# Kernel tuning notes

Hardware: AMD Instinct MI355X
Metric: run time of the kernel (lower is better)

The kernel has to match this reference:

```python
import jax, jax.numpy as jnp
import numpy as np

B, T, D = 2, 2048, 1024
K, F = 8, 4096
LAMBDA = 0.5


def setup_inputs() -> dict:
    key = jax.random.key(0)
    ks = jax.random.split(key, 8)
    s = 0.02
    return {
        "x": jax.random.normal(ks[0], (B, T, D), dtype=jnp.float32),
        "prev_logits": jax.random.normal(ks[1], (B, T, K), dtype=jnp.float32),
        "Wt": jax.random.normal(ks[2], (D, K), dtype=jnp.float32) * s,
        "Wgt": jax.random.normal(ks[3], (K, K), dtype=jnp.float32) * s,
        "We_logits": jnp.zeros((K,), dtype=jnp.float32),
        "W1": jax.random.normal(ks[4], (K, D, F), dtype=jnp.float32) * s,
        "b1": jnp.zeros((K, F), dtype=jnp.float32),
        "W2": jax.random.normal(ks[5], (K, F, D), dtype=jnp.float32) * s,
        "b2": jnp.zeros((K, D), dtype=jnp.float32),
    }


def reference(x, prev_logits, Wt, Wgt, We_logits, W1, b1, W2, b2):
    # gating: softmax over router logits, sigmoid-threshold multi-hot mask
    logits = jnp.einsum("btd,dk->btk", x, Wt) + jnp.einsum("btk,kj->btj", prev_logits, Wgt)
    st = jax.nn.softmax(logits, axis=-1)                       # (B,T,K)
    We = jax.nn.sigmoid(We_logits)                             # (K,)
    mask = (st > LAMBDA * We).astype(x.dtype)                  # (B,T,K)
    g = st * mask
    sel_counts = mask.sum(axis=(0, 1))                         # (K,)
    avg_density = mask.sum(axis=-1).mean()                     # scalar

    # dense multi-expert FFN: every expert on every token (dropout=0 / eval)
    h = jax.nn.gelu(jnp.einsum("btd,kdf->bktf", x, W1) + b1[:, None, :], approximate=False)
    outk = jnp.einsum("bktf,kfd->bktd", h, W2) + b2[:, None, :]  # (B,K,T,D)
    y = jnp.einsum("btk,bktd->btd", g, outk)
    y = y / (g.sum(axis=-1, keepdims=True) + 1e-6)
    return y, jax.lax.stop_gradient(logits), sel_counts, avg_density
```

## Files before the change

kernel.cpp:

```cpp
#include <hip/hip_runtime.h>
#include <cstdint>
#include <cstddef>

#define NB 2
#define NTT 2048
#define ND 1024
#define NK 8
#define NF 4096
#define NTOK (NB*NTT)
#define LAMBDA_C 0.5f

#define Y_SZ   (NTOK*ND)
#define LG_OFF Y_SZ
#define SC_OFF (LG_OFF + NTOK*NK)
#define AD_OFF (SC_OFF + NK)

#define WS_CNT    0
#define WS_SEG    8
#define WS_NTILES 17
#define WS_TILEK  32
#define WS_TILER  1056
#define WS_PTOK   4096
#define WS_PCOEF  36864
#define WS_COEF   69632
#define WS_X16    102400
#define B_X16   409600ull
#define B_W1T   8798208ull
#define B_W2T   75907072ull
#define B_HBUFN 143015936ull
#define B_HBUFF 8798208ull

#define BM 128
#define BN 64
#define BK 64
#define SPLITK2 4
#define KT 16

#define AOFF0 0u
#define AOFF1 16384u
#define BOFF0 32768u
#define BOFF1 40960u

typedef float  f32x4 __attribute__((ext_vector_type(4)));
typedef _Float16 f16x8 __attribute__((ext_vector_type(8)));
typedef unsigned int u32x2 __attribute__((ext_vector_type(2)));
typedef unsigned int u32x4 __attribute__((ext_vector_type(4)));

__device__ __forceinline__ unsigned int pkrtz(float a, float b){
    auto h = __builtin_amdgcn_cvt_pkrtz(a, b);
    return __builtin_bit_cast(unsigned int, h);
}
__device__ __forceinline__ float gelu_exact(float v){
    return 0.5f * v * (1.0f + erff(v * 0.70710678118654752440f));
}

__global__ __launch_bounds__(256) void k_xcast(const float* __restrict__ x,
                                               unsigned short* __restrict__ x16)
{
    int i = (blockIdx.x*256 + threadIdx.x) * 16;
    const f32x4* src = (const f32x4*)(x + i);
    f32x4 v0 = src[0], v1 = src[1], v2 = src[2], v3 = src[3];
    u32x4 o0 = {pkrtz(v0[0],v0[1]), pkrtz(v0[2],v0[3]), pkrtz(v1[0],v1[1]), pkrtz(v1[2],v1[3])};
    u32x4 o1 = {pkrtz(v2[0],v2[1]), pkrtz(v2[2],v2[3]), pkrtz(v3[0],v3[1]), pkrtz(v3[2],v3[3])};
    *(u32x4*)(x16 + i)     = o0;
    *(u32x4*)(x16 + i + 8) = o1;
}

__global__ __launch_bounds__(256) void k_wtrans(
    const float* __restrict__ W1, const float* __restrict__ W2,
    unsigned short* __restrict__ W1T, unsigned short* __restrict__ W2T)
{
    __shared__ char LT[8192];
    int b = blockIdx.x;
    const float* src; unsigned short* dst; int sld, dld;
    if (b < 8192){
        int k = b >> 10, dt = (b >> 6) & 15, ft = b & 63;
        src = W1 + ((size_t)k*ND + dt*64)*NF + ft*64; sld = NF;
        dst = W1T + ((size_t)k*NF + ft*64)*ND + dt*64; dld = ND;
    } else {
        int b2 = b - 8192;
        int k = b2 >> 10, ft = (b2 >> 4) & 63, dt = b2 & 15;
        src = W2 + ((size_t)k*NF + ft*64)*ND + dt*64; sld = ND;
        dst = W2T + ((size_t)k*ND + dt*64)*NF + ft*64; dld = NF;
    }
    int t = threadIdx.x;
    int rg = t >> 4, cg = t & 15;
    f32x4 v[4];
    #pragma unroll
    for (int i = 0; i < 4; i++) v[i] = *(const f32x4*)(src + (size_t)(rg*4+i)*sld + cg*4);
    unsigned wA[4], wB[4];
    #pragma unroll
    for (int r = 0; r < 4; r++){
        wA[r] = pkrtz(v[r][0], v[r][1]);
        wB[r] = pkrtz(v[r][2], v[r][3]);
    }
    #pragma unroll
    for (int j = 0; j < 4; j++){
        unsigned s0 = (j < 2) ? wA[1] : wB[1];
        unsigned s1 = (j < 2) ? wA[0] : wB[0];
        unsigned s2 = (j < 2) ? wA[3] : wB[3];
        unsigned s3 = (j < 2) ? wA[2] : wB[2];
        unsigned sel = (j & 1) ? 0x07060302u : 0x05040100u;
        unsigned o0 = __builtin_amdgcn_perm(s0, s1, sel);
        unsigned o1 = __builtin_amdgcn_perm(s2, s3, sel);
        unsigned row_ = (unsigned)(cg*4 + j);
        unsigned g_ = ((unsigned)rg) ^ (2u*(row_ & 7u));
        *(u32x2*)(&LT[row_*128u + g_*8u]) = (u32x2){o0, o1};
    }
    __syncthreads();
    int c = t >> 2, ch = t & 3;
    unsigned sfx = (unsigned)c & 7u;
    unsigned p0 = ((unsigned)(2*ch))     ^ sfx;
    unsigned p1 = ((unsigned)(2*ch + 1)) ^ sfx;
    u32x4 r0 = *(const u32x4*)(&LT[(unsigned)c*128u + p0*16u]);
    u32x4 r1 = *(const u32x4*)(&LT[(unsigned)c*128u + p1*16u]);
    unsigned short* dp = dst + (size_t)c*dld + ch*16;
    *(u32x4*)(dp)     = r0;
    *(u32x4*)(dp + 8) = r1;
}

__global__ __launch_bounds__(256) void k_gating(
    const float* __restrict__ x, const float* __restrict__ pl,
    const float* __restrict__ Wt, const float* __restrict__ Wgt,
    const float* __restrict__ Wel, float* __restrict__ out,
    float* __restrict__ coef, int* __restrict__ cnt)
{
    int t = blockIdx.x;
    const float* xt = x + (size_t)t * ND;
    float acc[NK] = {0,0,0,0,0,0,0,0};
    for (int d = threadIdx.x; d < ND; d += 256){
        float xv = xt[d];
        const float4* w = (const float4*)(Wt + (size_t)d * NK);
        float4 w0 = w[0], w1 = w[1];
        acc[0] += xv*w0.x; acc[1] += xv*w0.y; acc[2] += xv*w0.z; acc[3] += xv*w0.w;
        acc[4] += xv*w1.x; acc[5] += xv*w1.y; acc[6] += xv*w1.z; acc[7] += xv*w1.w;
    }
    __shared__ float red[4][NK];
    #pragma unroll
    for (int k = 0; k < NK; k++){
        float v = acc[k];
        #pragma unroll
        for (int off = 32; off; off >>= 1) v += __shfl_down(v, off);
        if ((threadIdx.x & 63) == 0) red[threadIdx.x >> 6][k] = v;
    }
    __syncthreads();
    if (threadIdx.x == 0){
        const float* p = pl + (size_t)t * NK;
        float pv[NK];
        #pragma unroll
        for (int j = 0; j < NK; j++) pv[j] = p[j];
        float lg[NK]; float mx = -1e30f;
        #pragma unroll
        for (int k = 0; k < NK; k++){
            float v = red[0][k] + red[1][k] + red[2][k] + red[3][k];
            #pragma unroll
            for (int j = 0; j < NK; j++) v += pv[j] * Wgt[j*NK + k];
            lg[k] = v; mx = fmaxf(mx, v);
            out[LG_OFF + (size_t)t*NK + k] = v;
        }
        float e[NK]; float s = 0.f;
        #pragma unroll
        for (int k = 0; k < NK; k++){ e[k] = expf(lg[k] - mx); s += e[k]; }
        float g[NK]; float gsum = 0.f;
        #pragma unroll
        for (int k = 0; k < NK; k++){
            float st = e[k] / s;
            float we = 1.f / (1.f + expf(-Wel[k]));
            bool m = st > LAMBDA_C * we;
            g[k] = m ? st : 0.f;
            gsum += g[k];
        }
        float inv = 1.f / (gsum + 1e-6f);
        #pragma unroll
        for (int k = 0; k < NK; k++){
            coef[(size_t)t*NK + k] = g[k] * inv;
            if (g[k] > 0.f) atomicAdd(&cnt[k], 1);
        }
    }
}

__global__ __launch_bounds__(256) void k_scan(
    const float* __restrict__ coef, int* __restrict__ wsi,
    float* __restrict__ wsf, int pair_cap)
{
    int k = blockIdx.x;
    const int* cnt = wsi + WS_CNT;
    int base = 0;
    for (int j = 0; j < k; j++) base += cnt[j];
    int tid = threadIdx.x, lane = tid & 63, w = tid >> 6;
    __shared__ int wsum[4];
    __shared__ int sbase;
    if (tid == 0){
        sbase = base;
        wsi[WS_SEG + k] = base;
        if (k == NK-1) wsi[WS_SEG + NK] = base + cnt[k];
    }
    __syncthreads();
    int* ptok = wsi + WS_PTOK;
    float* pc = wsf + WS_PCOEF;
    for (int c0 = 0; c0 < NTOK; c0 += 256){
        int t = c0 + tid;
        float c = coef[(size_t)t*NK + k];
        bool m = c > 0.f;
        unsigned long long bal = __ballot(m);
        int pre = __popcll(bal & ((1ull << lane) - 1ull));
        if (lane == 0) wsum[w] = __popcll(bal);
        __syncthreads();
        int b = sbase;
        for (int j = 0; j < w; j++) b += wsum[j];
        if (m){
            int pos = b + pre;
            if (pos < pair_cap){ ptok[pos] = t; pc[pos] = c; }
        }
        __syncthreads();
        if (tid == 0) sbase += wsum[0] + wsum[1] + wsum[2] + wsum[3];
        __syncthreads();
    }
}

__global__ void k_tiles(int* __restrict__ wsi, float* __restrict__ out, int pair_cap)
{
    if (threadIdx.x == 0 && blockIdx.x == 0){
        const int* cnt = wsi + WS_CNT;
        const int* seg = wsi + WS_SEG;
        int total = 0;
        for (int k = 0; k < NK; k++){ total += cnt[k]; out[SC_OFF + k] = (float)cnt[k]; }
        out[AD_OFF] = (float)total / (float)NTOK;
        int nt = 0;
        for (int k = 0; k < NK; k++){
            int e = min(seg[k+1], pair_cap);
            for (int r = seg[k]; r < e; r += BM){
                wsi[WS_TILEK + nt] = k; wsi[WS_TILER + nt] = r; nt++;
            }
        }
        wsi[WS_NTILES] = nt;
    }
}

#define XCD_PART_LOOP(nwork)                                              \
    int q_ = (nwork) >> 3, rr_ = (nwork) & 7;                             \
    int xcd_ = blockIdx.x & 7;                                            \
    int slot_ = blockIdx.x >> 3;                                          \
    int nslot_ = gridDim.x >> 3;                                          \
    int cntw_ = q_ + (xcd_ < rr_ ? 1 : 0);                                \
    int start_ = xcd_ * q_ + (xcd_ < rr_ ? xcd_ : rr_);                   \
    for (int p_ = slot_; p_ < cntw_; p_ += nslot_)


#define GLLN(aP0_, aP1_, bP0_, bP1_, t_, slot_)                           \
  { unsigned ab_ = (unsigned)(slot_)*16384u + (unsigned)(wv*1024);        \
    __builtin_amdgcn_global_load_lds(                                     \
        (const __attribute__((address_space(1))) void*)((aP0_) + (size_t)(t_)*32), \
        (__attribute__((address_space(3))) void*)(&lds[ab_]), 16, 0, 0);  \
    __builtin_amdgcn_global_load_lds(                                     \
        (const __attribute__((address_space(1))) void*)((aP1_) + (size_t)(t_)*32), \
        (__attribute__((address_space(3))) void*)(&lds[ab_ + 4096u]), 16, 0, 0); \
    __builtin_amdgcn_global_load_lds(                                     \
        (const __attribute__((address_space(1))) void*)((bP0_) + (size_t)(t_)*32), \
        (__attribute__((address_space(3))) void*)(&lds[ab_ + 8192u]), 16, 0, 0); \
    __builtin_amdgcn_global_load_lds(                                     \
        (const __attribute__((address_space(1))) void*)((bP1_) + (size_t)(t_)*32), \
        (__attribute__((address_space(3))) void*)(&lds[ab_ + 12288u]), 16, 0, 0); }

#define MFMAN(slot_)                                                      \
  { unsigned ab_ = (unsigned)(slot_)*16384u, bb_ = ab_ + 8192u;           \
    f16x8 af_[4], bf_[4];                                                 \
    _Pragma("unroll")                                                     \
    for (int m_ = 0; m_ < 4; m_++) af_[m_] = *(const f16x8*)(&lds[ab_ + aoff[m_]]); \
    _Pragma("unroll")                                                     \
    for (int n_ = 0; n_ < 4; n_++) bf_[n_] = *(const f16x8*)(&lds[bb_ + boff[n_]]); \
    __builtin_amdgcn_s_setprio(1);                                        \
    _Pragma("unroll")                                                     \
    for (int m_ = 0; m_ < 4; m_++)                                        \
    _Pragma("unroll")                                                     \
    for (int n_ = 0; n_ < 4; n_++)                                        \
        acc[m_][n_] = __builtin_amdgcn_mfma_f32_16x16x32_f16(af_[m_], bf_[n_], acc[m_][n_], 0, 0, 0); \
    __builtin_amdgcn_s_setprio(0); }

#define PIPE_N(APREF0_, APREF1_, BPREF0_, BPREF1_)                        \
    GLLN(APREF0_, APREF1_, BPREF0_, BPREF1_, 0, 0)                        \
    GLLN(APREF0_, APREF1_, BPREF0_, BPREF1_, 1, 1)                        \
    asm volatile("s_waitcnt vmcnt(4)" ::: "memory");                      \
    __builtin_amdgcn_s_barrier();                                         \
    __builtin_amdgcn_sched_barrier(0);                                    \
    for (int t = 0; t < 32; t++){                                         \
        int sl = t % 3;                                                   \
        if (t + 2 < 32){                                                  \
            GLLN(APREF0_, APREF1_, BPREF0_, BPREF1_, t+2, (t+2)%3)        \
            MFMAN(sl)                                                     \
            asm volatile("s_waitcnt vmcnt(4)" ::: "memory");              \
            __builtin_amdgcn_s_barrier();                                 \
            __builtin_amdgcn_sched_barrier(0);                            \
        } else if (t + 1 < 32){                                           \
            MFMAN(sl)                                                     \
            asm volatile("s_waitcnt vmcnt(0)" ::: "memory");              \
            __builtin_amdgcn_s_barrier();                                 \
            __builtin_amdgcn_sched_barrier(0);                            \
        } else {                                                          \
            MFMAN(sl)                                                     \
        }                                                                 \
    }

#define GEMMN_PRE()                                                       \
    int tid = threadIdx.x;                                                \
    int L = tid & 63;                                                     \
    int wv = tid >> 6;                                                    \
    int wr = wv >> 1, wc = wv & 1;                                        \
    int l15 = L & 15, q = L >> 4;                                         \
    unsigned aoff[4], boff[4];                                            \
    _Pragma("unroll")                                                     \
    for (int m_ = 0; m_ < 4; m_++){                                       \
        int r_ = wr*64 + m_*16 + l15;                                     \
        aoff[m_] = (unsigned)(r_*64) + ((unsigned)((q ^ r_) & 3) << 4);   \
    }                                                                     \
    _Pragma("unroll")                                                     \
    for (int n_ = 0; n_ < 4; n_++){                                       \
        int c_ = wc*64 + n_*16 + l15;                                     \
        boff[n_] = (unsigned)(c_*64) + ((unsigned)((q ^ c_) & 3) << 4);   \
    }                                                                     \
    int grow0 = wv*16 + (L >> 2);                                         \
    int grow1 = (4 + wv)*16 + (L >> 2);                                   \
    int qg8 = (((L & 3) ^ ((L >> 2) & 3))) * 8;

__global__ __launch_bounds__(256, 3) void k_gemm1n(
    const unsigned short* __restrict__ x16, const unsigned short* __restrict__ w1t,
    const float* __restrict__ b1, const int* __restrict__ wsi,
    unsigned short* __restrict__ hbuf, int pair_cap)
{
    __shared__ char lds[49152];
    __shared__ int stok[BM];
    const int* seg  = wsi + WS_SEG;
    const int* tk   = wsi + WS_TILEK;
    const int* tr   = wsi + WS_TILER;
    const int* ptok = wsi + WS_PTOK;
    int ntm = wsi[WS_NTILES];
    int nwork = ntm * (NF / 128);
    GEMMN_PRE()

    XCD_PART_LOOP(nwork){
        int widx = start_ + p_;
        int mt = widx % ntm;
        int ft = widx / ntm;
        int kexp = tk[mt];
        int row0 = tr[mt];
        int nrows = min(BM, seg[kexp+1] - row0);
        int f0 = ft * 128;
        __syncthreads();
        if (tid < BM){
            int r = row0 + tid;
            stok[tid] = (tid < nrows && r < pair_cap) ? ptok[r] : ptok[row0];
        }
        __syncthreads();
        const unsigned short* a0 = x16 + (size_t)stok[grow0]*ND + qg8;
        const unsigned short* a1 = x16 + (size_t)stok[grow1]*ND + qg8;
        const unsigned short* bb = w1t + (size_t)kexp*NF*ND;
        const unsigned short* b0 = bb + (size_t)(f0 + grow0)*ND + qg8;
        const unsigned short* b1p = bb + (size_t)(f0 + grow1)*ND + qg8;
        f32x4 acc[4][4] = {};
        PIPE_N(a0, a1, b0, b1p)
        const float* b1k = b1 + (size_t)kexp*NF;
        #pragma unroll
        for (int n = 0; n < 4; n++){
            int f = f0 + wc*64 + n*16 + l15;
            float bv = b1k[f];
            #pragma unroll
            for (int m = 0; m < 4; m++){
                int rl = wr*64 + m*16 + q*4;
                #pragma unroll
                for (int i = 0; i < 4; i++){
                    int r = rl + i;
                    if (r < nrows && row0 + r < pair_cap){
                        float v = gelu_exact(acc[m][n][i] + bv);
                        hbuf[(size_t)(row0+r)*NF + f] = (unsigned short)(pkrtz(v, 0.f) & 0xffffu);
                    }
                }
            }
        }
    }
}

__global__ __launch_bounds__(256, 3) void k_gemm2n(
    const unsigned short* __restrict__ hbuf, const unsigned short* __restrict__ w2t,
    const float* __restrict__ b2, const int* __restrict__ wsi,
    const float* __restrict__ wsf, float* __restrict__ out, int pair_cap)
{
    __shared__ char lds[49152];
    __shared__ int stok[BM];
    __shared__ float scoef[BM];
    const int* seg  = wsi + WS_SEG;
    const int* tk   = wsi + WS_TILEK;
    const int* tr   = wsi + WS_TILER;
    const int* ptok = wsi + WS_PTOK;
    const float* pcoef = wsf + WS_PCOEF;
    int ntm = wsi[WS_NTILES];
    int nwork = ntm * (ND / 128) * SPLITK2;
    GEMMN_PRE()

    XCD_PART_LOOP(nwork){
        int widx = start_ + p_;
        int mt = widx % ntm;
        int rest = widx / ntm;
        int dt = rest & 7;
        int spk = rest >> 3;
        int kexp = tk[mt];
        int row0 = tr[mt];
        int nrows = min(BM, seg[kexp+1] - row0);
        int d0 = dt * 128;
        __syncthreads();
        if (tid < BM){
            int r = row0 + tid;
            bool v = (tid < nrows && r < pair_cap);
            stok[tid]  = v ? ptok[r] : 0;
            scoef[tid] = v ? pcoef[r] : 0.f;
        }
        __syncthreads();
        int ar0 = row0 + grow0; if (ar0 >= pair_cap) ar0 = pair_cap - 1;
        int ar1 = row0 + grow1; if (ar1 >= pair_cap) ar1 = pair_cap - 1;
        const unsigned short* a0 = hbuf + (size_t)ar0*NF + spk*(NF/SPLITK2) + qg8;
        const unsigned short* a1 = hbuf + (size_t)ar1*NF + spk*(NF/SPLITK2) + qg8;
        const unsigned short* bb = w2t + (size_t)kexp*ND*NF + spk*(NF/SPLITK2);
        const unsigned short* b0 = bb + (size_t)(d0 + grow0)*NF + qg8;
        const unsigned short* b1p = bb + (size_t)(d0 + grow1)*NF + qg8;
        f32x4 acc[4][4] = {};
        PIPE_N(a0, a1, b0, b1p)
        const float* b2k = b2 + (size_t)kexp*ND;
        #pragma unroll
        for (int n = 0; n < 4; n++){
            int d = d0 + wc*64 + n*16 + l15;
            float bv = (spk == 0) ? b2k[d] : 0.f;
            #pragma unroll
            for (int m = 0; m < 4; m++){
                int rl = wr*64 + m*16 + q*4;
                #pragma unroll
                for (int i = 0; i < 4; i++){
                    int r = rl + i;
                    if (r < nrows && row0 + r < pair_cap){
                        float c = scoef[r];
                        atomicAdd(&out[(size_t)stok[r]*ND + d], c * (acc[m][n][i] + bv));
                    }
                }
            }
        }
    }
}

#define LOAD_A(dst_, tt_)                                                 \
    { const unsigned short* an_ = asrc + (tt_)*BK;                        \
      _Pragma("unroll")                                                   \
      for (int j_ = 0; j_ < 4; j_++) dst_[j_] = *(const u32x4*)(an_ + j_*8); }

#define LOAD_B(dst_, tt_, LDW_)                                           \
    { const float* bn_ = bsrc + (size_t)((tt_)*BK + bkq*4)*LDW_;          \
      _Pragma("unroll")                                                   \
      for (int r_ = 0; r_ < 4; r_++) dst_[r_] = *(const f32x4*)(bn_ + (size_t)r_*LDW_); }

#define STAGE_A(src_, AO_)                                                \
    { _Pragma("unroll")                                                   \
      for (int j_ = 0; j_ < 4; j_++){                                     \
          unsigned off_ = (AO_) + (unsigned)arow*128u +                   \
              ((((unsigned)(ahalf*4 + j_)) ^ (unsigned)(arow & 7)) << 4); \
          *(u32x4*)(&lds[off_]) = src_[j_];                               \
      } }

#define STAGE_B(src_, BO_)                                                \
    { unsigned wA_[4], wB_[4];                                            \
      _Pragma("unroll")                                                   \
      for (int r_ = 0; r_ < 4; r_++){                                     \
          wA_[r_] = pkrtz(src_[r_][0], src_[r_][1]);                      \
          wB_[r_] = pkrtz(src_[r_][2], src_[r_][3]);                      \
      }                                                                   \
      _Pragma("unroll")                                                   \
      for (int j_ = 0; j_ < 4; j_++){                                     \
          unsigned s0_ = (j_ < 2) ? wA_[1] : wB_[1];                      \
          unsigned s1_ = (j_ < 2) ? wA_[0] : wB_[0];                      \
          unsigned s2_ = (j_ < 2) ? wA_[3] : wB_[3];                      \
          unsigned s3_ = (j_ < 2) ? wA_[2] : wB_[2];                      \
          unsigned sel_ = (j_ & 1) ? 0x07060302u : 0x05040100u;           \
          unsigned o0_ = __builtin_amdgcn_perm(s0_, s1_, sel_);           \
          unsigned o1_ = __builtin_amdgcn_perm(s2_, s3_, sel_);           \
          unsigned col_ = (unsigned)(bcc*4 + j_);                         \
          unsigned off_ = (BO_) + col_*128u +                             \
              (((unsigned)(bkq*8)) ^ ((col_ & 7u) << 4));                 \
          *(u32x2*)(&lds[off_]) = (u32x2){o0_, o1_};                      \
      } }

#define MFMA_RD(AO_, BO_)                                                 \
    { __builtin_amdgcn_s_setprio(1);                                      \
      _Pragma("unroll")                                                   \
      for (int kk_ = 0; kk_ < 2; kk_++){                                  \
          unsigned sb_ = ((unsigned)(kk_*64 + q*16)) ^ swzL;              \
          f16x8 af_[4], bf_[2];                                           \
          _Pragma("unroll")                                               \
          for (int m_ = 0; m_ < 4; m_++)                                  \
              af_[m_] = *(const f16x8*)(&lds[(AO_) + (unsigned)(wr*64 + m_*16 + l15)*128u + sb_]); \
          _Pragma("unroll")                                               \
          for (int n_ = 0; n_ < 2; n_++)                                  \
              bf_[n_] = *(const f16x8*)(&lds[(BO_) + (unsigned)(wc*32 + n_*16 + l15)*128u + sb_]); \
          _Pragma("unroll")                                               \
          for (int m_ = 0; m_ < 4; m_++)                                  \
          _Pragma("unroll")                                               \
          for (int n_ = 0; n_ < 2; n_++)                                  \
              acc[m_][n_] = __builtin_amdgcn_mfma_f32_16x16x32_f16(af_[m_], bf_[n_], acc[m_][n_], 0, 0, 0); \
      }                                                                   \
      __builtin_amdgcn_s_setprio(0); }

#define STEP_SYNC()                                                       \
    asm volatile("s_waitcnt lgkmcnt(0)" ::: "memory");                    \
    __builtin_amdgcn_s_barrier();                                         \
    __builtin_amdgcn_sched_barrier(0);

__global__ __launch_bounds__(256, 3) void k_gemm1f(
    const unsigned short* __restrict__ x16, const float* __restrict__ W1,
    const float* __restrict__ b1, const int* __restrict__ wsi,
    unsigned short* __restrict__ hbuf, int pair_cap)
{
    __shared__ char lds[49152];
    __shared__ int stok[BM];
    const int* seg  = wsi + WS_SEG;
    const int* tk   = wsi + WS_TILEK;
    const int* tr   = wsi + WS_TILER;
    const int* ptok = wsi + WS_PTOK;
    int ntm = wsi[WS_NTILES];
    int nwork = ntm * (NF / BN);
    int tid  = threadIdx.x;
    int lane = tid & 63;
    int w    = tid >> 6;
    int wr = w >> 1, wc = w & 1;
    int l15 = lane & 15, q = lane >> 4;
    unsigned swzL = (unsigned)((l15 & 7) << 4);
    int arow = tid >> 1, ahalf = tid & 1;
    int bkq = tid >> 4, bcc = tid & 15;

    XCD_PART_LOOP(nwork){
        int widx = start_ + p_;
        int mt = widx % ntm;
        int ft = widx / ntm;
        int kexp = tk[mt];
        int row0 = tr[mt];
        int nrows = min(BM, seg[kexp+1] - row0);
        int f0 = ft * BN;
        __syncthreads();
        if (tid < BM){
            int r = row0 + tid;
            stok[tid] = (tid < nrows && r < pair_cap) ? ptok[r] : ptok[row0];
        }
        __syncthreads();
        const unsigned short* asrc = x16 + (size_t)stok[arow]*ND + ahalf*32;
        const float* bsrc = W1 + (size_t)kexp*ND*NF + f0 + bcc*4;
        u32x4 ga0[4], ga1[4]; f32x4 gb0[4], gb1[4];
        LOAD_A(ga0, 0) LOAD_B(gb0, 0, NF)
        LOAD_A(ga1, 1) LOAD_B(gb1, 1, NF)
        f32x4 acc[4][2] = {};
        for (int t = 0; t < KT; t += 2){
            STAGE_A(ga0, AOFF0) STAGE_B(gb0, BOFF0)
            if (t + 2 < KT){ LOAD_A(ga0, t+2) LOAD_B(gb0, t+2, NF) }
            STEP_SYNC()
            MFMA_RD(AOFF0, BOFF0)
            STAGE_A(ga1, AOFF1) STAGE_B(gb1, BOFF1)
            if (t + 3 < KT){ LOAD_A(ga1, t+3) LOAD_B(gb1, t+3, NF) }
            STEP_SYNC()
            MFMA_RD(AOFF1, BOFF1)
        }
        const float* b1k = b1 + (size_t)kexp*NF;
        #pragma unroll
        for (int n = 0; n < 2; n++){
            int f = f0 + wc*32 + n*16 + l15;
            float bv = b1k[f];
            #pragma unroll
            for (int m = 0; m < 4; m++){
                int rl = wr*64 + m*16 + q*4;
                #pragma unroll
                for (int i = 0; i < 4; i++){
                    int r = rl + i;
                    if (r < nrows && row0 + r < pair_cap){
                        float v = gelu_exact(acc[m][n][i] + bv);
                        hbuf[(size_t)(row0+r)*NF + f] = (unsigned short)(pkrtz(v, 0.f) & 0xffffu);
                    }
                }
            }
        }
    }
}

__global__ __launch_bounds__(256, 3) void k_gemm2f(
    const unsigned short* __restrict__ hbuf, const float* __restrict__ W2,
    const float* __restrict__ b2, const int* __restrict__ wsi,
    const float* __restrict__ wsf, float* __restrict__ out, int pair_cap)
{
    __shared__ char lds[49152];
    __shared__ int stok[BM];
    __shared__ float scoef[BM];
    const int* seg  = wsi + WS_SEG;
    const int* tk   = wsi + WS_TILEK;
    const int* tr   = wsi + WS_TILER;
    const int* ptok = wsi + WS_PTOK;
    const float* pcoef = wsf + WS_PCOEF;
    int ntm = wsi[WS_NTILES];
    int nwork = ntm * (ND / BN) * SPLITK2;
    int tid  = threadIdx.x;
    int lane = tid & 63;
    int w    = tid >> 6;
    int wr = w >> 1, wc = w & 1;
    int l15 = lane & 15, q = lane >> 4;
    unsigned swzL = (unsigned)((l15 & 7) << 4);
    int arow = tid >> 1, ahalf = tid & 1;
    int bkq = tid >> 4, bcc = tid & 15;

    XCD_PART_LOOP(nwork){
        int widx = start_ + p_;
        int mt = widx % ntm;
        int rest = widx / ntm;
        int dt = rest & 15;
        int sp = rest >> 4;
        int kexp = tk[mt];
        int row0 = tr[mt];
        int nrows = min(BM, seg[kexp+1] - row0);
        int d0 = dt * BN;
        __syncthreads();
        if (tid < BM){
            int r = row0 + tid;
            bool v = (tid < nrows && r < pair_cap);
            stok[tid]  = v ? ptok[r] : 0;
            scoef[tid] = v ? pcoef[r] : 0.f;
        }
        __syncthreads();
        int hr = row0 + arow; if (hr >= pair_cap) hr = pair_cap - 1;
        const unsigned short* asrc = hbuf + (size_t)hr*NF + sp*(NF/SPLITK2) + ahalf*32;
        const float* bsrc = W2 + (size_t)kexp*NF*ND + (size_t)sp*(NF/SPLITK2)*ND + d0 + bcc*4;
        u32x4 ga0[4], ga1[4]; f32x4 gb0[4], gb1[4];
        LOAD_A(ga0, 0) LOAD_B(gb0, 0, ND)
        LOAD_A(ga1, 1) LOAD_B(gb1, 1, ND)
        f32x4 acc[4][2] = {};
        for (int t = 0; t < KT; t += 2){
            STAGE_A(ga0, AOFF0) STAGE_B(gb0, BOFF0)
            if (t + 2 < KT){ LOAD_A(ga0, t+2) LOAD_B(gb0, t+2, ND) }
            STEP_SYNC()
            MFMA_RD(AOFF0, BOFF0)
            STAGE_A(ga1, AOFF1) STAGE_B(gb1, BOFF1)
            if (t + 3 < KT){ LOAD_A(ga1, t+3) LOAD_B(gb1, t+3, ND) }
            STEP_SYNC()
            MFMA_RD(AOFF1, BOFF1)
        }
        const float* b2k = b2 + (size_t)kexp*ND;
        #pragma unroll
        for (int n = 0; n < 2; n++){
            int d = d0 + wc*32 + n*16 + l15;
            float bv = (sp == 0) ? b2k[d] : 0.f;
            #pragma unroll
            for (int m = 0; m < 4; m++){
                int rl = wr*64 + m*16 + q*4;
                #pragma unroll
                for (int i = 0; i < 4; i++){
                    int r = rl + i;
                    if (r < nrows && row0 + r < pair_cap){
                        float c = scoef[r];
                        atomicAdd(&out[(size_t)stok[r]*ND + d], c * (acc[m][n][i] + bv));
                    }
                }
            }
        }
    }
}

extern "C" void kernel_launch(void* const* d_in, const int* in_sizes, int n_in,
                              void* d_out, int out_size, void* d_ws, size_t ws_size,
                              hipStream_t stream)
{
    const float* x   = (const float*)d_in[0];
    const float* pl  = (const float*)d_in[1];
    const float* Wt  = (const float*)d_in[2];
    const float* Wgt = (const float*)d_in[3];
    const float* Wel = (const float*)d_in[4];
    const float* W1  = (const float*)d_in[5];
    const float* b1  = (const float*)d_in[6];
    const float* W2  = (const float*)d_in[7];
    const float* b2  = (const float*)d_in[8];
    float* out = (float*)d_out;
    int* wsi   = (int*)d_ws;
    float* wsf = (float*)d_ws;
    unsigned short* x16 = (unsigned short*)((char*)d_ws + B_X16);

    long long capn = ((long long)ws_size - (long long)B_HBUFN) / ((long long)NF*2);
    bool newpath = capn >= 4096;

    hipMemsetAsync(d_out, 0, (size_t)out_size*sizeof(float), stream);
    hipMemsetAsync(d_ws, 0, 32, stream);
    k_xcast<<<1024, 256, 0, stream>>>(x, x16);
    k_gating<<<NTOK, 256, 0, stream>>>(x, pl, Wt, Wgt, Wel, out, wsf + WS_COEF, wsi + WS_CNT);

    if (newpath){
        unsigned short* w1t  = (unsigned short*)((char*)d_ws + B_W1T);
        unsigned short* w2t  = (unsigned short*)((char*)d_ws + B_W2T);
        unsigned short* hbuf = (unsigned short*)((char*)d_ws + B_HBUFN);
        int pair_cap = (int)((capn > 32768) ? 32768 : capn);
        k_wtrans<<<16384, 256, 0, stream>>>(W1, W2, w1t, w2t);
        k_scan<<<NK, 256, 0, stream>>>(wsf + WS_COEF, wsi, wsf, pair_cap);
        k_tiles<<<1, 64, 0, stream>>>(wsi, out, pair_cap);
        k_gemm1n<<<2048, 256, 0, stream>>>(x16, w1t, b1, wsi, hbuf, pair_cap);
        k_gemm2n<<<2048, 256, 0, stream>>>(hbuf, w2t, b2, wsi, wsf, out, pair_cap);
    } else {
        unsigned short* hbuf = (unsigned short*)((char*)d_ws + B_HBUFF);
        long long cap = ((long long)ws_size - (long long)B_HBUFF) / ((long long)NF*2);
        if (cap > (long long)NTOK*NK) cap = (long long)NTOK*NK;
        if (cap < 0) cap = 0;
        int pair_cap = (int)cap;
        if (pair_cap > 0){
            k_scan<<<NK, 256, 0, stream>>>(wsf + WS_COEF, wsi, wsf, pair_cap);
            k_tiles<<<1, 64, 0, stream>>>(wsi, out, pair_cap);
            k_gemm1f<<<2048, 256, 0, stream>>>(x16, W1, b1, wsi, hbuf, pair_cap);
            k_gemm2f<<<2048, 256, 0, stream>>>(hbuf, W2, b2, wsi, wsf, out, pair_cap);
        }
    }
}
```

Measured before the change: 270.2 us.

## Fuse x fp16 cast into gating, stage GEMM1 epilogue through LDS, reswizzle transpose

Removes the separate x-to-fp16 cast kernel and does the conversion inside the gating kernel, which already reads each token row. This saves one launch and one extra read of x. The GEMM1 epilogue now writes GELU results into a swizzled LDS tile and stores full 16-byte vectors per row to hbuf, replacing scattered 2-byte global stores. The weight-transpose LDS swizzle keys are also changed to reduce bank conflicts. The staging adds two barriers and reuses the pipeline LDS, which relies on the 128x128 fp16 tile fitting in the 48KB buffer.

```diff
diff --git a/kernel.cpp b/kernel.cpp
--- a/kernel.cpp
+++ b/kernel.cpp
@@ -54,18 +54,6 @@
     return 0.5f * v * (1.0f + erff(v * 0.70710678118654752440f));
 }
 
-__global__ __launch_bounds__(256) void k_xcast(const float* __restrict__ x,
-                                               unsigned short* __restrict__ x16)
-{
-    int i = (blockIdx.x*256 + threadIdx.x) * 16;
-    const f32x4* src = (const f32x4*)(x + i);
-    f32x4 v0 = src[0], v1 = src[1], v2 = src[2], v3 = src[3];
-    u32x4 o0 = {pkrtz(v0[0],v0[1]), pkrtz(v0[2],v0[3]), pkrtz(v1[0],v1[1]), pkrtz(v1[2],v1[3])};
-    u32x4 o1 = {pkrtz(v2[0],v2[1]), pkrtz(v2[2],v2[3]), pkrtz(v3[0],v3[1]), pkrtz(v3[2],v3[3])};
-    *(u32x4*)(x16 + i)     = o0;
-    *(u32x4*)(x16 + i + 8) = o1;
-}
-
 __global__ __launch_bounds__(256) void k_wtrans(
     const float* __restrict__ W1, const float* __restrict__ W2,
     unsigned short* __restrict__ W1T, unsigned short* __restrict__ W2T)
@@ -104,14 +92,14 @@
         unsigned o0 = __builtin_amdgcn_perm(s0, s1, sel);
         unsigned o1 = __builtin_amdgcn_perm(s2, s3, sel);
         unsigned row_ = (unsigned)(cg*4 + j);
-        unsigned g_ = ((unsigned)rg) ^ (2u*(row_ & 7u));
+        unsigned g_ = ((unsigned)rg) ^ (((row_ >> 2) & 3u) << 2);
         *(u32x2*)(&LT[row_*128u + g_*8u]) = (u32x2){o0, o1};
     }
     __syncthreads();
     int c = t >> 2, ch = t & 3;
-    unsigned sfx = (unsigned)c & 7u;
-    unsigned p0 = ((unsigned)(2*ch))     ^ sfx;
-    unsigned p1 = ((unsigned)(2*ch + 1)) ^ sfx;
+    unsigned key16 = (((unsigned)c >> 2) & 3u) << 1;
+    unsigned p0 = ((unsigned)(2*ch))     ^ key16;
+    unsigned p1 = ((unsigned)(2*ch + 1)) ^ key16;
     u32x4 r0 = *(const u32x4*)(&LT[(unsigned)c*128u + p0*16u]);
     u32x4 r1 = *(const u32x4*)(&LT[(unsigned)c*128u + p1*16u]);
     unsigned short* dp = dst + (size_t)c*dld + ch*16;
@@ -123,7 +111,8 @@
     const float* __restrict__ x, const float* __restrict__ pl,
     const float* __restrict__ Wt, const float* __restrict__ Wgt,
     const float* __restrict__ Wel, float* __restrict__ out,
-    float* __restrict__ coef, int* __restrict__ cnt)
+    float* __restrict__ coef, int* __restrict__ cnt,
+    unsigned short* __restrict__ x16)
 {
     int t = blockIdx.x;
     const float* xt = x + (size_t)t * ND;
@@ -134,6 +123,12 @@
         float4 w0 = w[0], w1 = w[1];
         acc[0] += xv*w0.x; acc[1] += xv*w0.y; acc[2] += xv*w0.z; acc[3] += xv*w0.w;
         acc[4] += xv*w1.x; acc[5] += xv*w1.y; acc[6] += xv*w1.z; acc[7] += xv*w1.w;
+    }
+    {
+        int i4 = threadIdx.x * 4;
+        f32x4 xv = *(const f32x4*)(xt + i4);
+        u32x2 o = {pkrtz(xv[0], xv[1]), pkrtz(xv[2], xv[3])};
+        *(u32x2*)(x16 + (size_t)t*ND + i4) = o;
     }
     __shared__ float red[4][NK];
     #pragma unroll
@@ -245,7 +240,6 @@
     int cntw_ = q_ + (xcd_ < rr_ ? 1 : 0);                                \
     int start_ = xcd_ * q_ + (xcd_ < rr_ ? xcd_ : rr_);                   \
     for (int p_ = slot_; p_ < cntw_; p_ += nslot_)
-
 
 #define GLLN(aP0_, aP1_, bP0_, bP1_, t_, slot_)                           \
   { unsigned ab_ = (unsigned)(slot_)*16384u + (unsigned)(wv*1024);        \
@@ -358,21 +352,35 @@
         const unsigned short* b1p = bb + (size_t)(f0 + grow1)*ND + qg8;
         f32x4 acc[4][4] = {};
         PIPE_N(a0, a1, b0, b1p)
+        __syncthreads();
         const float* b1k = b1 + (size_t)kexp*NF;
         #pragma unroll
         for (int n = 0; n < 4; n++){
-            int f = f0 + wc*64 + n*16 + l15;
-            float bv = b1k[f];
+            int fl = wc*64 + n*16 + l15;
+            float bv = b1k[f0 + fl];
+            unsigned col2 = (unsigned)fl * 2u;
             #pragma unroll
             for (int m = 0; m < 4; m++){
-                int rl = wr*64 + m*16 + q*4;
+                int rb = wr*64 + m*16 + q*4;
                 #pragma unroll
                 for (int i = 0; i < 4; i++){
-                    int r = rl + i;
-                    if (r < nrows && row0 + r < pair_cap){
-                        float v = gelu_exact(acc[m][n][i] + bv);
-                        hbuf[(size_t)(row0+r)*NF + f] = (unsigned short)(pkrtz(v, 0.f) & 0xffffu);
-                    }
+                    int r = rb + i;
+                    float v = gelu_exact(acc[m][n][i] + bv);
+                    unsigned short hv = (unsigned short)(pkrtz(v, 0.f) & 0xffffu);
+                    unsigned pp = (col2 >> 4) ^ ((unsigned)r & 15u);
+                    *(unsigned short*)(&lds[(unsigned)r*256u + pp*16u + (col2 & 15u)]) = hv;
+                }
+            }
+        }
+        __syncthreads();
+        {
+            int r = tid >> 1, half = tid & 1;
+            if (r < nrows && row0 + r < pair_cap){
+                unsigned short* dp = hbuf + (size_t)(row0+r)*NF + f0 + half*64;
+                #pragma unroll
+                for (int j = 0; j < 8; j++){
+                    unsigned pp = ((unsigned)(half*8 + j)) ^ ((unsigned)r & 15u);
+                    *(u32x4*)(dp + j*8) = *(const u32x4*)(&lds[(unsigned)r*256u + pp*16u]);
                 }
             }
         }
@@ -685,8 +693,7 @@
 
     hipMemsetAsync(d_out, 0, (size_t)out_size*sizeof(float), stream);
     hipMemsetAsync(d_ws, 0, 32, stream);
-    k_xcast<<<1024, 256, 0, stream>>>(x, x16);
-    k_gating<<<NTOK, 256, 0, stream>>>(x, pl, Wt, Wgt, Wel, out, wsf + WS_COEF, wsi + WS_CNT);
+    k_gating<<<NTOK, 256, 0, stream>>>(x, pl, Wt, Wgt, Wel, out, wsf + WS_COEF, wsi + WS_CNT, x16);
 
     if (newpath){
         unsigned short* w1t  = (unsigned short*)((char*)d_ws + B_W1T);
```

Result: faster. 261.3 us (-3.3%).
